# Kernel optimization log

Measured on AMD Instinct MI355X. Metric: run time of the kernel, lower is better.

Reference implementation:

```python
import jax, jax.numpy as jnp
import numpy as np

SQRT2 = 1.4142135623730951  # fused_leaky_relu gain
DN = ('NCHW', 'OIHW', 'NCHW')


def _setup_filter():
    # upfirdn2d.setup_filter([1,3,3,1]): separable outer product, normalized to sum 1
    f = jnp.array([1., 3., 3., 1.], dtype=jnp.float32)
    f = f / jnp.sum(f)
    return jnp.outer(f, f)  # [4,4], symmetric so flip is a no-op


def _depthwise_fir(x, f2, pad, down):
    # upfirdn2d: depthwise conv with the 4x4 resample filter
    C = x.shape[1]
    k = jnp.broadcast_to(f2[None, None], (C, 1, 4, 4)).astype(x.dtype)
    return jax.lax.conv_general_dilated(
        x, k, window_strides=(down, down),
        padding=[(pad, pad), (pad, pad)],
        feature_group_count=C, dimension_numbers=DN)


def _conv(x, w, stride, pad):
    return jax.lax.conv_general_dilated(
        x, w, window_strides=(stride, stride),
        padding=[(pad, pad), (pad, pad)], dimension_numbers=DN)


def _act(x):
    # fused_leaky_relu with no bias: leaky_relu(x, 0.2) * sqrt(2)
    return jax.nn.leaky_relu(x, negative_slope=0.2) * SQRT2


def setup_inputs() -> dict:
    key = jax.random.key(0)
    k1, k2, k3, k4 = jax.random.split(key, 4)
    N, Cin, Cout, H = 16, 256, 512, 64
    return {
        'latents_in': jax.random.normal(k1, (N, Cin, H, H), dtype=jnp.float32),
        'w_conv': jax.random.normal(k2, (Cin, Cin, 3, 3), dtype=jnp.float32),
        'w_down': jax.random.normal(k3, (Cout, Cin, 3, 3), dtype=jnp.float32),
        'w_skip': jax.random.normal(k4, (Cout, Cin, 1, 1), dtype=jnp.float32),
    }


def reference(latents_in, w_conv, w_down, w_skip):
    f2 = _setup_filter()
    Cin = w_conv.shape[1]
    g3 = 1.0 / np.sqrt(Cin * 9)   # weight_gain for 3x3 convs
    g1 = 1.0 / np.sqrt(Cin)       # weight_gain for 1x1 skip conv

    y = latents_in
    # self.conv: 3x3, pad 1, stride 1, no bias, fused leaky relu
    x = _act(_conv(y, w_conv * g3, stride=1, pad=1))
    # self.conv_down: FIR lowpass (pad 2) then 3x3 conv stride 2 (conv2d_resample down=2)
    x = _depthwise_fir(x, f2, pad=2, down=1)          # [N,Cin,H+1,H+1]
    out = _act(_conv(x, w_down * g3, stride=2, pad=0))  # [N,Cout,H/2,H/2]
    # skip path: downsample2d(y) then 1x1 conv (no bias) + act
    skip = _depthwise_fir(y, f2, pad=1, down=2)       # [N,Cin,H/2,H/2]
    skip = _act(_conv(skip, w_skip * g1, stride=1, pad=0))
    return skip + out
```

## Files before the change

kernel.cpp:

```cpp
#include <hip/hip_runtime.h>
#include <hip/hip_bf16.h>
#include <stdint.h>


typedef __bf16 bf8v __attribute__((ext_vector_type(8)));
typedef float  f4   __attribute__((ext_vector_type(4)));

#define G3F (1.0f / 48.0f)
#define G1F (1.0f / 16.0f)
#define SQRT2F 1.4142135623730951f

__device__ __forceinline__ float actf(float v) {
    return (v > 0.0f ? v : 0.2f * v) * SQRT2F;
}
__device__ __forceinline__ unsigned short f2bu(float f) {
    __hip_bfloat16 h = __float2bfloat16(f);
    return *reinterpret_cast<unsigned short*>(&h);
}
__device__ __forceinline__ bf8v ld8(const __hip_bfloat16* p) {
    return *reinterpret_cast<const bf8v*>(p);
}
__device__ __forceinline__ void llds16(const __hip_bfloat16* g, void* l) {
    __builtin_amdgcn_global_load_lds(
        (const __attribute__((address_space(1))) unsigned int*)g,
        (__attribute__((address_space(3))) unsigned int*)l, 16, 0, 0);
}

__global__ __launch_bounds__(256) void p_pad(__hip_bfloat16* __restrict__ xb,
                                             __hip_bfloat16* __restrict__ zbuf) {
    int idx = blockIdx.x * 256 + threadIdx.x;
    int c8 = idx & 31, side = (idx >> 5) & 1, h = (idx >> 6) & 63, n = idx >> 12;
    int wp = side * 65;
    uint4 z = {0, 0, 0, 0};
    *reinterpret_cast<uint4*>(xb + (((size_t)(n * 64 + h) * 66 + wp) << 8) + c8 * 8) = z;
    if (blockIdx.x == 0 && threadIdx.x < 64)
        *reinterpret_cast<uint4*>(zbuf + (threadIdx.x << 3)) = z;
}

__global__ __launch_bounds__(256) void p_xb(const float* __restrict__ lat,
                                            __hip_bfloat16* __restrict__ xb) {
    __shared__ float tile[32][65];
    int bx = blockIdx.x;
    int cic = bx & 7, h = (bx >> 3) & 63, n = bx >> 9;
    int ci0 = cic * 32;
    int t = threadIdx.x;
    {
        int cir = t >> 3, wq = (t & 7) * 8;
        const float* src = lat + (((size_t)(n * 256 + ci0 + cir) * 64 + h) * 64 + wq);
        float4 v0 = *(const float4*)src;
        float4 v1 = *(const float4*)(src + 4);
        tile[cir][wq + 0] = v0.x; tile[cir][wq + 1] = v0.y;
        tile[cir][wq + 2] = v0.z; tile[cir][wq + 3] = v0.w;
        tile[cir][wq + 4] = v1.x; tile[cir][wq + 5] = v1.y;
        tile[cir][wq + 6] = v1.z; tile[cir][wq + 7] = v1.w;
    }
    __syncthreads();
    {
        int w = t >> 2, c8 = (t & 3) * 8;
        union { uint4 q; unsigned short h8[8]; } pk;
        #pragma unroll
        for (int j = 0; j < 8; ++j) pk.h8[j] = f2bu(tile[c8 + j][w]);
        __hip_bfloat16* dst = xb + (((size_t)(n * 64 + h) * 66 + (w + 1)) << 8) + ci0 + c8;
        *reinterpret_cast<uint4*>(dst) = pk.q;
    }
}

__global__ __launch_bounds__(256) void p_wA(const float* __restrict__ w,
                                            __hip_bfloat16* __restrict__ wA) {
    int idx = blockIdx.x * 256 + threadIdx.x;
    int lane = idx & 63;
    int co16 = (idx >> 6) & 15;
    int q    = (idx >> 10) & 7;
    int t    = idx >> 13;
    int co = co16 * 16 + (lane & 15);
    int ci = q * 32 + (lane >> 4) * 8;
    union { uint4 v; unsigned short h8[8]; } pk;
    #pragma unroll
    for (int e = 0; e < 8; ++e)
        pk.h8[e] = f2bu(w[(size_t)(co * 256 + ci + e) * 9 + t] * G3F);
    *reinterpret_cast<uint4*>(wA + (size_t)idx * 8) = pk.v;
}
__global__ __launch_bounds__(256) void p_wD(const float* __restrict__ w,
                                            __hip_bfloat16* __restrict__ wD) {
    int idx = blockIdx.x * 256 + threadIdx.x;
    int lane = idx & 63;
    int co16 = (idx >> 6) & 31;
    int q    = (idx >> 11) & 7;
    int t    = idx >> 14;
    int co = co16 * 16 + (lane & 15);
    int ci = q * 32 + (lane >> 4) * 8;
    union { uint4 v; unsigned short h8[8]; } pk;
    #pragma unroll
    for (int e = 0; e < 8; ++e)
        pk.h8[e] = f2bu(w[(size_t)(co * 256 + ci + e) * 9 + t] * G3F);
    *reinterpret_cast<uint4*>(wD + (size_t)idx * 8) = pk.v;
}
__global__ __launch_bounds__(256) void p_ws(const float* __restrict__ w,
                                            __hip_bfloat16* __restrict__ wst) {
    int idx = blockIdx.x * 256 + threadIdx.x;
    wst[idx] = __float2bfloat16(w[idx] * G1F);
}

__global__ __launch_bounds__(256) void k_fir2n(const __hip_bfloat16* __restrict__ xb,
                                               __hip_bfloat16* __restrict__ s2) {
    int idx = blockIdx.x * 256 + threadIdx.x;
    int c8 = idx & 31, ow = (idx >> 5) & 31, oh = (idx >> 10) & 31, n = idx >> 15;
    const float fk[4] = {0.125f, 0.375f, 0.375f, 0.125f};
    float a8[8];
    #pragma unroll
    for (int e = 0; e < 8; ++e) a8[e] = 0.0f;
    const __hip_bfloat16* src = xb + ((size_t)n * 64 * 66) * 256 + c8 * 8;
    #pragma unroll
    for (int i = 0; i < 4; ++i) {
        int rr = 2 * oh + i - 1;
        if ((unsigned)rr >= 64u) continue;
        #pragma unroll
        for (int j = 0; j < 4; ++j) {
            int wp = 2 * ow + j;
            bf8v v = ld8(src + ((size_t)(rr * 66 + wp) << 8));
            float fw = fk[i] * fk[j];
            #pragma unroll
            for (int e = 0; e < 8; ++e) a8[e] += fw * (float)v[e];
        }
    }
    union { uint4 q; unsigned short h8[8]; } pk;
    #pragma unroll
    for (int e = 0; e < 8; ++e) pk.h8[e] = f2bu(a8[e]);
    *reinterpret_cast<uint4*>(s2 + (((size_t)(n * 1024 + oh * 32 + ow)) << 8) + c8 * 8) = pk.q;
}

__global__ __launch_bounds__(256) void k_skipg(const __hip_bfloat16* __restrict__ s2,
                                               const __hip_bfloat16* __restrict__ wst,
                                               float* __restrict__ out) {
    const int lane = threadIdx.x & 63;
    const int wid  = threadIdx.x >> 6;
    const int wr = wid & 1, wc = wid >> 1;
    const int l15 = lane & 15, g = lane >> 4;

    int raw = blockIdx.x;
    int lg  = (raw & 7) * 64 + (raw >> 3);
    int cot = lg >> 7, pxt = lg & 127;
    int n = pxt >> 3, oh0 = (pxt & 7) * 4;

    f4 acc[4][4];
    #pragma unroll
    for (int m = 0; m < 4; ++m)
        #pragma unroll
        for (int nf = 0; nf < 4; ++nf)
            #pragma unroll
            for (int e = 0; e < 4; ++e) acc[m][nf][e] = 0.0f;

    #pragma unroll
    for (int k = 0; k < 8; ++k) {
        bf8v a_[4], b_[4];
        #pragma unroll
        for (int nf = 0; nf < 4; ++nf) {
            int oh = oh0 + wc * 2 + (nf >> 1);
            int ow = (nf & 1) * 16 + l15;
            b_[nf] = ld8(s2 + (((size_t)(n * 1024 + oh * 32 + ow)) << 8) + k * 32 + g * 8);
        }
        #pragma unroll
        for (int m = 0; m < 4; ++m) {
            int co = cot * 128 + wr * 64 + m * 16 + l15;
            a_[m] = ld8(wst + (size_t)co * 256 + k * 32 + g * 8);
        }
        #pragma unroll
        for (int m = 0; m < 4; ++m)
            #pragma unroll
            for (int nf = 0; nf < 4; ++nf)
                acc[m][nf] = __builtin_amdgcn_mfma_f32_16x16x32_bf16(
                    a_[m], b_[nf], acc[m][nf], 0, 0, 0);
    }
    #pragma unroll
    for (int m = 0; m < 4; ++m)
        #pragma unroll
        for (int nf = 0; nf < 4; ++nf) {
            f4 v = acc[m][nf];
            int oh = oh0 + wc * 2 + (nf >> 1);
            int ow = (nf & 1) * 16 + l15;
            int co = cot * 128 + wr * 64 + m * 16 + 4 * g;
            #pragma unroll
            for (int r = 0; r < 4; ++r)
                out[((size_t)(n * 512 + co + r)) * 1024 + oh * 32 + ow] = actf(v[r]);
        }
}

__global__ __launch_bounds__(256, 4) void k_conv1s(const __hip_bfloat16* __restrict__ xb,
                                                   const __hip_bfloat16* __restrict__ wA,
                                                   const __hip_bfloat16* __restrict__ zbuf,
                                                   __hip_bfloat16* __restrict__ x1) {
    __shared__ uint4 smq[2112];
    char* smc = (char*)smq;
    const int tid  = threadIdx.x;
    const int lane = tid & 63;
    const int wid  = tid >> 6;
    const int wr = wid & 1, wc = wid >> 1;
    const int l15 = lane & 15, g = lane >> 4;

    int raw = blockIdx.x;
    int lg  = (raw & 7) * 128 + (raw >> 3);
    int cot = lg >> 9, pxt = lg & 511;
    int n = pxt >> 5, h0 = (pxt & 31) * 2;
    const size_t nb66 = (size_t)n * 64 * 66 * 256;
    const size_t nb   = (size_t)n * 4096 * 256;
    const char* wAc = (const char*)wA;

    f4 acc[4][4];
    #pragma unroll
    for (int m = 0; m < 4; ++m)
        #pragma unroll
        for (int nf = 0; nf < 4; ++nf)
            #pragma unroll
            for (int e = 0; e < 4; ++e) acc[m][nf][e] = 0.0f;

    #pragma unroll 1
    for (int ch = 0; ch < 4; ++ch) {
        if (ch) __syncthreads();
        for (int li = wid; li < 33; li += 4) {
            int gi = li * 64 + lane;
            int row = (gi >= 1584) ? 3 : (gi >= 1056) ? 2 : (gi >= 528) ? 1 : 0;
            int rem = gi - row * 528;
            int wp = rem >> 3;
            int c8 = (rem & 7) ^ (wp & 7);
            int rc = h0 - 1 + row;
            const __hip_bfloat16* src = ((unsigned)rc < 64u)
                ? xb + nb66 + (((size_t)(rc * 66 + wp)) << 8) + ch * 64 + c8 * 8
                : zbuf + (lane << 3);
            llds16(src, smc + li * 1024);
        }
        __syncthreads();

        #pragma unroll
        for (int kh = 0; kh < 3; ++kh) {
            #pragma unroll
            for (int kw = 0; kw < 3; ++kw) {
                #pragma unroll
                for (int qq = 0; qq < 2; ++qq) {
                    int c8r = qq * 4 + g;
                    bf8v b_[4];
                    #pragma unroll
                    for (int nf = 0; nf < 4; ++nf) {
                        int wp = nf * 16 + l15 + kw;
                        int off = (wc + kh) * 8448 + (wp * 8 + (c8r ^ (wp & 7))) * 16;
                        b_[nf] = *(const bf8v*)(smc + off);
                    }
                    int q = ch * 2 + qq;
                    #pragma unroll
                    for (int m = 0; m < 4; ++m) {
                        bf8v a = *(const bf8v*)(wAc +
                            ((size_t)(((kh * 3 + kw) * 8 + q) * 16 + cot * 8 + wr * 4 + m) << 10) +
                            (lane << 4));
                        #pragma unroll
                        for (int nf = 0; nf < 4; ++nf)
                            acc[m][nf] = __builtin_amdgcn_mfma_f32_16x16x32_bf16(
                                a, b_[nf], acc[m][nf], 0, 0, 0);
                    }
                }
            }
        }
    }

    __syncthreads();
    #pragma unroll
    for (int m = 0; m < 4; ++m)
        #pragma unroll
        for (int nf = 0; nf < 4; ++nf) {
            int p = wc * 64 + nf * 16 + l15;
            int co4 = wr * 16 + m * 4 + g;
            int co4s = co4 ^ ((p & 15) << 1);
            union { unsigned long long u; unsigned short h4[4]; } pk;
            #pragma unroll
            for (int r = 0; r < 4; ++r) pk.h4[r] = f2bu(actf(acc[m][nf][r]));
            *reinterpret_cast<unsigned long long*>(smc + p * 256 + co4s * 8) = pk.u;
        }
    __syncthreads();
    {
        int p = tid >> 1, coh = tid & 1;
        int hh = h0 + (p >> 6), w = p & 63;
        __hip_bfloat16* dst = x1 + nb + (((size_t)(hh * 64 + w)) << 8) + cot * 128 + coh * 64;
        #pragma unroll
        for (int j = 0; j < 8; ++j) {
            int r2 = coh * 8 + j;
            int co4s = (2 * r2) ^ ((p & 15) << 1);
            uint4 v = *reinterpret_cast<const uint4*>(smc + p * 256 + co4s * 8);
            *reinterpret_cast<uint4*>(dst + j * 8) = v;
        }
    }
}

__global__ __launch_bounds__(256) void k_fir1(const __hip_bfloat16* __restrict__ x1,
                                              __hip_bfloat16* __restrict__ xf) {
    int idx = blockIdx.x * 256 + threadIdx.x;
    int c8 = idx & 31; int rest = idx >> 5;
    int owq = rest % 17; rest /= 17;
    int oh = rest % 65; int n = rest / 65;
    int ow0 = owq * 4; if (ow0 > 61) ow0 = 61;
    int ci = c8 * 8;
    const float fk[4] = {0.125f, 0.375f, 0.375f, 0.125f};
    const __hip_bfloat16* src = x1 + (size_t)n * 4096 * 256 + ci;

    float t[7][8];
    #pragma unroll
    for (int c = 0; c < 7; ++c) {
        #pragma unroll
        for (int e = 0; e < 8; ++e) t[c][e] = 0.0f;
        int col = ow0 - 2 + c;
        if ((unsigned)col >= 64u) continue;
        #pragma unroll
        for (int i = 0; i < 4; ++i) {
            int r = oh + i - 2;
            if ((unsigned)r >= 64u) continue;
            bf8v v = ld8(src + ((size_t)(r * 64 + col) << 8));
            float fw = fk[i];
            #pragma unroll
            for (int e = 0; e < 8; ++e) t[c][e] += fw * (float)v[e];
        }
    }
    #pragma unroll
    for (int o = 0; o < 4; ++o) {
        union { uint4 q; unsigned short h8[8]; } pk;
        #pragma unroll
        for (int e = 0; e < 8; ++e) {
            float s = fk[0] * t[o][e] + fk[1] * t[o + 1][e] +
                      fk[2] * t[o + 2][e] + fk[3] * t[o + 3][e];
            pk.h8[e] = f2bu(s);
        }
        *reinterpret_cast<uint4*>(
            xf + ((size_t)n * 4225 + oh * 65 + ow0 + o) * 256 + ci) = pk.q;
    }
}

__global__ __launch_bounds__(256, 4) void k_downs(const __hip_bfloat16* __restrict__ xf,
                                                  const __hip_bfloat16* __restrict__ wD,
                                                  float* __restrict__ out) {
    __shared__ uint4 smq[1344];
    char* smc = (char*)smq;
    const int tid  = threadIdx.x;
    const int lane = tid & 63;
    const int wid  = tid >> 6;
    const int l15  = lane & 15, g = lane >> 4;

    int raw = blockIdx.x;
    int lg  = (raw & 7) * 128 + (raw >> 3);
    int cot = lg >> 8;
    int rest = lg & 255;
    int n = rest >> 4, oht = rest & 15;
    int r0 = oht * 4;
    const size_t nxf = (size_t)n * 4225 * 256;
    const char* wDc = (const char*)wD;

    f4 acc[2][4];
    #pragma unroll
    for (int m = 0; m < 2; ++m)
        #pragma unroll
        for (int nf = 0; nf < 4; ++nf)
            #pragma unroll
            for (int e = 0; e < 4; ++e) acc[m][nf][e] = 0.0f;

    #pragma unroll 1
    for (int ch = 0; ch < 8; ++ch) {
        if (ch) __syncthreads();
        for (int li = wid; li < 21; li += 4) {
            int gi = li * 64 + lane;
            if (gi > 1319) gi = 1319;
            int row = (gi >= 1056) ? 4 : (gi >= 792) ? 3 : (gi >= 528) ? 2 :
                      (gi >= 264) ? 1 : 0;
            int rem = gi - row * 264;
            int wpair = rem >> 3;
            int t4 = (rem & 7) ^ (wpair & 7);
            int odd = t4 >> 2, c8 = t4 & 3;
            int wp = wpair * 2 + odd; if (wp > 64) wp = 64;
            const __hip_bfloat16* src = xf + nxf +
                (((size_t)((r0 + row) * 65 + wp)) << 8) + ch * 32 + c8 * 8;
            llds16(src, smc + li * 1024);
        }
        __syncthreads();

        #pragma unroll
        for (int kh = 0; kh < 3; ++kh) {
            #pragma unroll
            for (int kw = 0; kw < 3; ++kw) {
                bf8v b_[4];
                #pragma unroll
                for (int nf = 0; nf < 4; ++nf) {
                    int ow = (nf & 1) * 16 + l15;
                    int wp = 2 * ow + kw;
                    int wpair = wp >> 1, odd = wp & 1;
                    int s8 = (g + 4 * odd) ^ (wpair & 7);
                    int off = ((2 * (nf >> 1) + kh) * 264 + wpair * 8 + s8) * 16;
                    b_[nf] = *(const bf8v*)(smc + off);
                }
                #pragma unroll
                for (int m = 0; m < 2; ++m) {
                    bf8v a = *(const bf8v*)(wDc +
                        ((size_t)(((kh * 3 + kw) * 8 + ch) * 32 + cot * 8 + wid * 2 + m) << 10) +
                        (lane << 4));
                    #pragma unroll
                    for (int nf = 0; nf < 4; ++nf)
                        acc[m][nf] = __builtin_amdgcn_mfma_f32_16x16x32_bf16(
                            a, b_[nf], acc[m][nf], 0, 0, 0);
                }
            }
        }
    }

    #pragma unroll
    for (int m = 0; m < 2; ++m)
        #pragma unroll
        for (int nf = 0; nf < 4; ++nf) {
            f4 v = acc[m][nf];
            int oh = oht * 2 + (nf >> 1);
            int ow = (nf & 1) * 16 + l15;
            int co = cot * 128 + wid * 32 + m * 16 + 4 * g;
            #pragma unroll
            for (int r = 0; r < 4; ++r) {
                size_t oi = ((size_t)(n * 512 + co + r)) * 1024 + oh * 32 + ow;
                out[oi] += actf(v[r]);
            }
        }
}

extern "C" void kernel_launch(void* const* d_in, const int* in_sizes, int n_in,
                              void* d_out, int out_size, void* d_ws, size_t ws_size,
                              hipStream_t stream) {
    const float* lat   = (const float*)d_in[0];
    const float* wconv = (const float*)d_in[1];
    const float* wdown = (const float*)d_in[2];
    const float* wskip = (const float*)d_in[3];
    float* out = (float*)d_out;

    char* base = (char*)d_ws;
    __hip_bfloat16* xb   = (__hip_bfloat16*)base;
    __hip_bfloat16* xf   = (__hip_bfloat16*)base;
    __hip_bfloat16* x1   = (__hip_bfloat16*)(base + 34611200);
    __hip_bfloat16* s2   = (__hip_bfloat16*)(base + 34611200);
    __hip_bfloat16* wA   = (__hip_bfloat16*)(base + 68165632);
    __hip_bfloat16* wD   = (__hip_bfloat16*)(base + 69345280);
    __hip_bfloat16* wst  = (__hip_bfloat16*)(base + 71704576);
    __hip_bfloat16* zbuf = (__hip_bfloat16*)(base + 71966720);

    hipLaunchKernelGGL(p_pad,   dim3(256),  dim3(256), 0, stream, xb, zbuf);
    hipLaunchKernelGGL(p_xb,    dim3(8192), dim3(256), 0, stream, lat,   xb);
    hipLaunchKernelGGL(p_wA,    dim3(288),  dim3(256), 0, stream, wconv, wA);
    hipLaunchKernelGGL(p_wD,    dim3(576),  dim3(256), 0, stream, wdown, wD);
    hipLaunchKernelGGL(p_ws,    dim3(512),  dim3(256), 0, stream, wskip, wst);
    hipLaunchKernelGGL(k_fir2n, dim3(2048), dim3(256), 0, stream, xb, s2);
    hipLaunchKernelGGL(k_skipg, dim3(512),  dim3(256), 0, stream, s2, wst, out);
    hipLaunchKernelGGL(k_conv1s, dim3(1024), dim3(256), 0, stream, xb, wA, zbuf, x1);
    hipLaunchKernelGGL(k_fir1,  dim3(2210), dim3(256), 0, stream, x1, xf);
    hipLaunchKernelGGL(k_downs, dim3(1024), dim3(256), 0, stream, xf, wD, out);
}
```

Before: 232.1 us.

## Software-pipeline MFMA operand loads in conv kernels and merge prep launches

```diff
diff --git a/kernel.cpp b/kernel.cpp
--- a/kernel.cpp
+++ b/kernel.cpp
@@ -26,15 +26,53 @@
         (__attribute__((address_space(3))) unsigned int*)l, 16, 0, 0);
 }
 
-__global__ __launch_bounds__(256) void p_pad(__hip_bfloat16* __restrict__ xb,
-                                             __hip_bfloat16* __restrict__ zbuf) {
-    int idx = blockIdx.x * 256 + threadIdx.x;
-    int c8 = idx & 31, side = (idx >> 5) & 1, h = (idx >> 6) & 63, n = idx >> 12;
-    int wp = side * 65;
-    uint4 z = {0, 0, 0, 0};
-    *reinterpret_cast<uint4*>(xb + (((size_t)(n * 64 + h) * 66 + wp) << 8) + c8 * 8) = z;
-    if (blockIdx.x == 0 && threadIdx.x < 64)
-        *reinterpret_cast<uint4*>(zbuf + (threadIdx.x << 3)) = z;
+__global__ __launch_bounds__(256) void p_misc(__hip_bfloat16* __restrict__ xb,
+                                              __hip_bfloat16* __restrict__ zbuf,
+                                              const float* __restrict__ wconv,
+                                              __hip_bfloat16* __restrict__ wA,
+                                              const float* __restrict__ wdown,
+                                              __hip_bfloat16* __restrict__ wD,
+                                              const float* __restrict__ wskip,
+                                              __hip_bfloat16* __restrict__ wst) {
+    int b = blockIdx.x, t = threadIdx.x;
+    if (b < 256) {
+        int idx = b * 256 + t;
+        int c8 = idx & 31, side = (idx >> 5) & 1, h = (idx >> 6) & 63, n = idx >> 12;
+        int wp = side * 65;
+        uint4 z = {0, 0, 0, 0};
+        *reinterpret_cast<uint4*>(xb + (((size_t)(n * 64 + h) * 66 + wp) << 8) + c8 * 8) = z;
+        if (b == 0 && t < 64)
+            *reinterpret_cast<uint4*>(zbuf + (t << 3)) = z;
+    } else if (b < 544) {
+        int idx = (b - 256) * 256 + t;
+        int lane = idx & 63;
+        int co16 = (idx >> 6) & 15;
+        int q    = (idx >> 10) & 7;
+        int tp   = idx >> 13;
+        int co = co16 * 16 + (lane & 15);
+        int ci = q * 32 + (lane >> 4) * 8;
+        union { uint4 v; unsigned short h8[8]; } pk;
+        #pragma unroll
+        for (int e = 0; e < 8; ++e)
+            pk.h8[e] = f2bu(wconv[(size_t)(co * 256 + ci + e) * 9 + tp] * G3F);
+        *reinterpret_cast<uint4*>(wA + (size_t)idx * 8) = pk.v;
+    } else if (b < 1120) {
+        int idx = (b - 544) * 256 + t;
+        int lane = idx & 63;
+        int co16 = (idx >> 6) & 31;
+        int q    = (idx >> 11) & 7;
+        int tp   = idx >> 14;
+        int co = co16 * 16 + (lane & 15);
+        int ci = q * 32 + (lane >> 4) * 8;
+        union { uint4 v; unsigned short h8[8]; } pk;
+        #pragma unroll
+        for (int e = 0; e < 8; ++e)
+            pk.h8[e] = f2bu(wdown[(size_t)(co * 256 + ci + e) * 9 + tp] * G3F);
+        *reinterpret_cast<uint4*>(wD + (size_t)idx * 8) = pk.v;
+    } else {
+        int idx = (b - 1120) * 256 + t;
+        wst[idx] = __float2bfloat16(wskip[idx] * G1F);
+    }
 }
 
 __global__ __launch_bounds__(256) void p_xb(const float* __restrict__ lat,
@@ -65,42 +103,6 @@
     }
 }
 
-__global__ __launch_bounds__(256) void p_wA(const float* __restrict__ w,
-                                            __hip_bfloat16* __restrict__ wA) {
-    int idx = blockIdx.x * 256 + threadIdx.x;
-    int lane = idx & 63;
-    int co16 = (idx >> 6) & 15;
-    int q    = (idx >> 10) & 7;
-    int t    = idx >> 13;
-    int co = co16 * 16 + (lane & 15);
-    int ci = q * 32 + (lane >> 4) * 8;
-    union { uint4 v; unsigned short h8[8]; } pk;
-    #pragma unroll
-    for (int e = 0; e < 8; ++e)
-        pk.h8[e] = f2bu(w[(size_t)(co * 256 + ci + e) * 9 + t] * G3F);
-    *reinterpret_cast<uint4*>(wA + (size_t)idx * 8) = pk.v;
-}
-__global__ __launch_bounds__(256) void p_wD(const float* __restrict__ w,
-                                            __hip_bfloat16* __restrict__ wD) {
-    int idx = blockIdx.x * 256 + threadIdx.x;
-    int lane = idx & 63;
-    int co16 = (idx >> 6) & 31;
-    int q    = (idx >> 11) & 7;
-    int t    = idx >> 14;
-    int co = co16 * 16 + (lane & 15);
-    int ci = q * 32 + (lane >> 4) * 8;
-    union { uint4 v; unsigned short h8[8]; } pk;
-    #pragma unroll
-    for (int e = 0; e < 8; ++e)
-        pk.h8[e] = f2bu(w[(size_t)(co * 256 + ci + e) * 9 + t] * G3F);
-    *reinterpret_cast<uint4*>(wD + (size_t)idx * 8) = pk.v;
-}
-__global__ __launch_bounds__(256) void p_ws(const float* __restrict__ w,
-                                            __hip_bfloat16* __restrict__ wst) {
-    int idx = blockIdx.x * 256 + threadIdx.x;
-    wst[idx] = __float2bfloat16(w[idx] * G1F);
-}
-
 __global__ __launch_bounds__(256) void k_fir2n(const __hip_bfloat16* __restrict__ xb,
                                                __hip_bfloat16* __restrict__ s2) {
     int idx = blockIdx.x * 256 + threadIdx.x;
@@ -230,33 +232,45 @@
         }
         __syncthreads();
 
-        #pragma unroll
-        for (int kh = 0; kh < 3; ++kh) {
-            #pragma unroll
-            for (int kw = 0; kw < 3; ++kw) {
+        auto loadBf = [&](int p, int nf) -> bf8v {
+            int tap = p >> 1, qq = p & 1;
+            int kh = tap / 3, kw = tap % 3;
+            int wp = nf * 16 + l15 + kw;
+            int c8r = qq * 4 + g;
+            int off = (wc + kh) * 8448 + (wp * 8 + (c8r ^ (wp & 7))) * 16;
+            return *(const bf8v*)(smc + off);
+        };
+        auto loadAf = [&](int p, int m) -> bf8v {
+            int tap = p >> 1, q = ch * 2 + (p & 1);
+            return *(const bf8v*)(wAc +
+                ((size_t)((tap * 8 + q) * 16 + cot * 8 + wr * 4 + m) << 10) +
+                (lane << 4));
+        };
+
+        bf8v aF[4], bF[4];
+        #pragma unroll
+        for (int nf = 0; nf < 4; ++nf) bF[nf] = loadBf(0, nf);
+        #pragma unroll
+        for (int m = 0; m < 4; ++m) aF[m] = loadAf(0, m);
+
+        #pragma unroll
+        for (int p = 0; p < 18; ++p) {
+            const bool lastp = (p == 17);
+            #pragma unroll
+            for (int m = 0; m < 3; ++m) {
                 #pragma unroll
-                for (int qq = 0; qq < 2; ++qq) {
-                    int c8r = qq * 4 + g;
-                    bf8v b_[4];
-                    #pragma unroll
-                    for (int nf = 0; nf < 4; ++nf) {
-                        int wp = nf * 16 + l15 + kw;
-                        int off = (wc + kh) * 8448 + (wp * 8 + (c8r ^ (wp & 7))) * 16;
-                        b_[nf] = *(const bf8v*)(smc + off);
-                    }
-                    int q = ch * 2 + qq;
-                    #pragma unroll
-                    for (int m = 0; m < 4; ++m) {
-                        bf8v a = *(const bf8v*)(wAc +
-                            ((size_t)(((kh * 3 + kw) * 8 + q) * 16 + cot * 8 + wr * 4 + m) << 10) +
-                            (lane << 4));
-                        #pragma unroll
-                        for (int nf = 0; nf < 4; ++nf)
-                            acc[m][nf] = __builtin_amdgcn_mfma_f32_16x16x32_bf16(
-                                a, b_[nf], acc[m][nf], 0, 0, 0);
-                    }
-                }
+                for (int nf = 0; nf < 4; ++nf)
+                    acc[m][nf] = __builtin_amdgcn_mfma_f32_16x16x32_bf16(
+                        aF[m], bF[nf], acc[m][nf], 0, 0, 0);
+                if (!lastp) aF[m] = loadAf(p + 1, m);
             }
+            #pragma unroll
+            for (int nf = 0; nf < 4; ++nf) {
+                acc[3][nf] = __builtin_amdgcn_mfma_f32_16x16x32_bf16(
+                    aF[3], bF[nf], acc[3][nf], 0, 0, 0);
+                if (!lastp) bF[nf] = loadBf(p + 1, nf);
+            }
+            if (!lastp) aF[3] = loadAf(p + 1, 3);
         }
     }
 
@@ -376,31 +390,42 @@
         }
         __syncthreads();
 
-        #pragma unroll
-        for (int kh = 0; kh < 3; ++kh) {
-            #pragma unroll
-            for (int kw = 0; kw < 3; ++kw) {
-                bf8v b_[4];
-                #pragma unroll
-                for (int nf = 0; nf < 4; ++nf) {
-                    int ow = (nf & 1) * 16 + l15;
-                    int wp = 2 * ow + kw;
-                    int wpair = wp >> 1, odd = wp & 1;
-                    int s8 = (g + 4 * odd) ^ (wpair & 7);
-                    int off = ((2 * (nf >> 1) + kh) * 264 + wpair * 8 + s8) * 16;
-                    b_[nf] = *(const bf8v*)(smc + off);
-                }
-                #pragma unroll
-                for (int m = 0; m < 2; ++m) {
-                    bf8v a = *(const bf8v*)(wDc +
-                        ((size_t)(((kh * 3 + kw) * 8 + ch) * 32 + cot * 8 + wid * 2 + m) << 10) +
-                        (lane << 4));
-                    #pragma unroll
-                    for (int nf = 0; nf < 4; ++nf)
-                        acc[m][nf] = __builtin_amdgcn_mfma_f32_16x16x32_bf16(
-                            a, b_[nf], acc[m][nf], 0, 0, 0);
-                }
+        auto loadBf = [&](int p, int nf) -> bf8v {
+            int kh = p / 3, kw = p % 3;
+            int ow = (nf & 1) * 16 + l15;
+            int wp = 2 * ow + kw;
+            int wpair = wp >> 1, odd = wp & 1;
+            int s8 = (g + 4 * odd) ^ (wpair & 7);
+            int off = ((2 * (nf >> 1) + kh) * 264 + wpair * 8 + s8) * 16;
+            return *(const bf8v*)(smc + off);
+        };
+        auto loadAf = [&](int p, int m) -> bf8v {
+            return *(const bf8v*)(wDc +
+                ((size_t)((p * 8 + ch) * 32 + cot * 8 + wid * 2 + m) << 10) +
+                (lane << 4));
+        };
+
+        bf8v aF[2], bF[4];
+        #pragma unroll
+        for (int nf = 0; nf < 4; ++nf) bF[nf] = loadBf(0, nf);
+        #pragma unroll
+        for (int m = 0; m < 2; ++m) aF[m] = loadAf(0, m);
+
+        #pragma unroll
+        for (int p = 0; p < 9; ++p) {
+            const bool lastp = (p == 8);
+            #pragma unroll
+            for (int nf = 0; nf < 4; ++nf)
+                acc[0][nf] = __builtin_amdgcn_mfma_f32_16x16x32_bf16(
+                    aF[0], bF[nf], acc[0][nf], 0, 0, 0);
+            if (!lastp) aF[0] = loadAf(p + 1, 0);
+            #pragma unroll
+            for (int nf = 0; nf < 4; ++nf) {
+                acc[1][nf] = __builtin_amdgcn_mfma_f32_16x16x32_bf16(
+                    aF[1], bF[nf], acc[1][nf], 0, 0, 0);
+                if (!lastp) bF[nf] = loadBf(p + 1, nf);
             }
+            if (!lastp) aF[1] = loadAf(p + 1, 1);
         }
     }
 
@@ -439,11 +464,9 @@
     __hip_bfloat16* wst  = (__hip_bfloat16*)(base + 71704576);
     __hip_bfloat16* zbuf = (__hip_bfloat16*)(base + 71966720);
 
-    hipLaunchKernelGGL(p_pad,   dim3(256),  dim3(256), 0, stream, xb, zbuf);
+    hipLaunchKernelGGL(p_misc, dim3(1632), dim3(256), 0, stream,
+                       xb, zbuf, wconv, wA, wdown, wD, wskip, wst);
     hipLaunchKernelGGL(p_xb,    dim3(8192), dim3(256), 0, stream, lat,   xb);
-    hipLaunchKernelGGL(p_wA,    dim3(288),  dim3(256), 0, stream, wconv, wA);
-    hipLaunchKernelGGL(p_wD,    dim3(576),  dim3(256), 0, stream, wdown, wD);
-    hipLaunchKernelGGL(p_ws,    dim3(512),  dim3(256), 0, stream, wskip, wst);
     hipLaunchKernelGGL(k_fir2n, dim3(2048), dim3(256), 0, stream, xb, s2);
     hipLaunchKernelGGL(k_skipg, dim3(512),  dim3(256), 0, stream, s2, wst, out);
     hipLaunchKernelGGL(k_conv1s, dim3(1024), dim3(256), 0, stream, xb, wA, zbuf, x1);
```

Result: slower. 241.1 us (+3.9%).
